# Kernel optimization log

Hardware: AMD Instinct MI355X
Metric: run time of the kernel (lower is better)

The kernel has to match this reference:

```python
import jax, jax.numpy as jnp
import numpy as np

N_NODES = 100000
N_EDGES = 1600000
DIM = 64


def setup_inputs() -> dict:
    key = jax.random.key(0)
    ks = jax.random.split(key, 10)
    return {
        "h_real": jax.random.normal(ks[0], (N_NODES, DIM), dtype=jnp.float32),
        "h_imag": jax.random.normal(ks[1], (N_NODES, DIM), dtype=jnp.float32),
        "d": jax.random.uniform(ks[2], (N_NODES,), dtype=jnp.float32),
        "w_real": jax.random.normal(ks[3], (N_EDGES,), dtype=jnp.float32),
        "w_imag": jax.random.normal(ks[4], (N_EDGES,), dtype=jnp.float32),
        "src": jax.random.randint(ks[5], (N_EDGES,), 0, N_NODES, dtype=jnp.int32),
        "dst": jax.random.randint(ks[6], (N_EDGES,), 0, N_NODES, dtype=jnp.int32),
        "W1": jax.random.normal(ks[7], (DIM, DIM), dtype=jnp.float32) * (1.414 / np.sqrt(DIM)),
        "b1": jnp.zeros((DIM,), dtype=jnp.float32),
        "W2": jax.random.normal(ks[8], (DIM, DIM), dtype=jnp.float32) * (1.414 / np.sqrt(DIM)),
        "b2": jnp.zeros((DIM,), dtype=jnp.float32),
    }


def reference(h_real, h_imag, d, w_real, w_imag, src, dst, W1, b1, W2, b2):
    n = h_real.shape[0]
    # per-edge complex coefficient e = d_dst * d_src * (w_real + i w_imag)
    dd = d[dst] * d[src]                      # [E]
    e_r = (dd * w_real)[:, None]              # [E,1]
    e_i = (dd * w_imag)[:, None]              # [E,1]
    hr = h_real[src]                          # [E,D]
    hi = h_imag[src]                          # [E,D]
    # complex multiply e * h, fused single pass over edges
    m_r = e_r * hr - e_i * hi                 # [E,D]
    m_i = e_i * hr + e_r * hi                 # [E,D]
    z_real = jax.ops.segment_sum(m_r, dst, num_segments=n)  # [N,D]
    z_imag = jax.ops.segment_sum(m_i, dst, num_segments=n)  # [N,D]
    # note: original overwrites z_real first, then z_imag uses the NEW z_real
    zr = (z_real @ W1.T + b1) - (z_imag @ W2.T + b2)
    zi = (zr @ W2.T + b2) + (z_imag @ W1.T + b1)
    return zr, zi
```

## Files before the change

### kernel.cpp

```cpp
#include <hip/hip_runtime.h>
#include <hip/hip_bf16.h>

#define N_NODES 100000
#define N_EDGES 1600000
#define DIM 64

#define K1 ((N_NODES + 255) / 256)
#define PACKB4 ((N_NODES * DIM / 4 + 255) / 256)
#define PTILE 8192
#define PARTB ((N_EDGES + PTILE - 1) / PTILE)
#define CAP 4480
#define QCAP 1344

typedef __attribute__((ext_vector_type(8))) short bf16x8;
typedef __attribute__((ext_vector_type(4))) float f32x4;

#if defined(__has_builtin)
#if __has_builtin(__builtin_amdgcn_fdot2_f32_bf16)
#define HAVE_DOT2 1
typedef __attribute__((ext_vector_type(2))) __bf16 bf16x2v;
#endif
#endif


__device__ __forceinline__ unsigned pack_bf16x2(float lo, float hi) {
  unsigned ulo = (unsigned)__hip_bfloat16_raw(__float2bfloat16(lo)).x;
  unsigned uhi = (unsigned)__hip_bfloat16_raw(__float2bfloat16(hi)).x;
  return ulo | (uhi << 16);
}
__device__ __forceinline__ float unpack_lo(unsigned u) {
  return __int_as_float((int)(u << 16));
}
__device__ __forceinline__ float unpack_hi(unsigned u) {
  return __int_as_float((int)(u & 0xFFFF0000u));
}
__device__ __forceinline__ unsigned short f2bf(float x) {
  return __hip_bfloat16_raw(__float2bfloat16(x)).x;
}

__global__ __launch_bounds__(256) void mega_kernel(
    const float* __restrict__ h_real, const float* __restrict__ h_imag,
    unsigned* __restrict__ hpack, const float* __restrict__ W1,
    const float* __restrict__ b1, const float* __restrict__ W2,
    const float* __restrict__ b2, unsigned short* __restrict__ At,
    float* __restrict__ cvec, const int* __restrict__ src,
    const int* __restrict__ dst, const float* __restrict__ dvec,
    const float* __restrict__ w_real, const float* __restrict__ w_imag,
    int* __restrict__ cursor, unsigned long long* __restrict__ records) {
  __shared__ __align__(16) float wstage[8192];
  const int bid = blockIdx.x;
  const int tid = threadIdx.x;

  if (bid < PACKB4) {
    const int i = bid * 256 + tid;
    const float4 hr = ((const float4*)h_real)[i];
    const float4 hi = ((const float4*)h_imag)[i];
    uint4 o;
    o.x = pack_bf16x2(hr.x, hi.x);
    o.y = pack_bf16x2(hr.y, hi.y);
    o.z = pack_bf16x2(hr.z, hi.z);
    o.w = pack_bf16x2(hr.w, hi.w);
    ((uint4*)hpack)[i] = o;
    return;
  }

  if (bid < PACKB4 + 64) {
    float* w1s = wstage;
    float* w2s = wstage + 4096;
    for (int i = tid; i < 64 * 64; i += 256) {
      w1s[i] = W1[i];
      w2s[i] = W2[i];
    }
    __syncthreads();
    const int idx = (bid - PACKB4) * 256 + tid;
    if (idx < 128 * 128) {
      const int n = idx >> 7, k = idx & 127;
      float v;
      if (n < 64) {
        v = (k < 64) ? w1s[n * 64 + k] : -w2s[n * 64 + (k - 64)];
      } else {
        const int nn = n - 64;
        if (k < 64) {
          float s = 0.0f;
          for (int j = 0; j < 64; ++j) s += w1s[j * 64 + k] * w2s[nn * 64 + j];
          v = s;
        } else {
          const int kk = k - 64;
          float s = 0.0f;
          for (int j = 0; j < 64; ++j) s += w2s[j * 64 + kk] * w2s[nn * 64 + j];
          v = w1s[nn * 64 + kk] - s;
        }
      }
      At[n * 128 + k] = f2bf(v);
    }
    if (idx < 128) {
      if (idx < 64) {
        cvec[idx] = b1[idx] - b2[idx];
      } else {
        const int nn = idx - 64;
        float s = 0.0f;
        for (int j = 0; j < 64; ++j) s += (b1[j] - b2[j]) * w2s[nn * 64 + j];
        cvec[idx] = s + b1[nn] + b2[nn];
      }
    }
    return;
  }

  int* lh = (int*)wstage;
  int* mybase = lh + K1;
  const int pb = bid - PACKB4 - 64;
  const int e0 = pb * PTILE;
  const int cnt_t = min(PTILE, N_EDGES - e0);

  for (int i = tid; i < K1; i += 256) lh[i] = 0;
  __syncthreads();

#pragma unroll
  for (int g = 0; g < PTILE / 1024; ++g) {
    const int off = g * 1024 + tid * 4;
    if (off < cnt_t) {
      const int4 t4 = *(const int4*)(dst + e0 + off);
      atomicAdd(&lh[t4.x >> 8], 1);
      atomicAdd(&lh[t4.y >> 8], 1);
      atomicAdd(&lh[t4.z >> 8], 1);
      atomicAdd(&lh[t4.w >> 8], 1);
    }
  }
  __syncthreads();

  for (int b = tid; b < K1; b += 256) {
    const int c = lh[b];
    mybase[b] = c ? atomicAdd(&cursor[b], c) : 0;
    lh[b] = 0;
  }
  __syncthreads();

#pragma unroll
  for (int g = 0; g < PTILE / 1024; ++g) {
    const int off = g * 1024 + tid * 4;
    if (off < cnt_t) {
      const int e = e0 + off;
      const int4 s4 = *(const int4*)(src + e);
      const int4 t4 = *(const int4*)(dst + e);
      const float4 wr = *(const float4*)(w_real + e);
      const float4 wi = *(const float4*)(w_imag + e);
#define EMIT(SS, TT, WR, WI)                                              \
      {                                                                   \
        const int b = (TT) >> 8;                                          \
        const float ds = dvec[SS];                                        \
        const unsigned lo = (unsigned)(SS) | ((unsigned)((TT) & 255) << 17); \
        const unsigned hi = pack_bf16x2(ds * (WR), ds * (WI));            \
        const int r = atomicAdd(&lh[b], 1);                               \
        const int pos = mybase[b] + r;                                    \
        if (pos < CAP)                                                    \
          records[(size_t)b * CAP + pos] =                                \
              ((unsigned long long)hi << 32) | lo;                        \
      }
      EMIT(s4.x, t4.x, wr.x, wi.x)
      EMIT(s4.y, t4.y, wr.y, wi.y)
      EMIT(s4.z, t4.z, wr.z, wi.z)
      EMIT(s4.w, t4.w, wr.w, wi.w)
#undef EMIT
    }
  }
}

__global__ __launch_bounds__(512, 8) void pull_sorted_kernel(
    const unsigned long long* __restrict__ records,
    const int* __restrict__ cursor, const float* __restrict__ dvec,
    const unsigned* __restrict__ hpack, const unsigned short* __restrict__ At,
    const float* __restrict__ cvec, float* __restrict__ zr_out,
    float* __restrict__ zi_out) {
  __shared__ unsigned long long stageB[QCAP];
  __shared__ __align__(16) unsigned short zs[64][136];
  __shared__ int ncnt[64];
  __shared__ int ncur[64];
  __shared__ int ns[64];
  __shared__ int ne[64];
  const int tid = threadIdx.x;
  const int lane = tid & 63;
  const int wave = tid >> 6;
  const int q4 = lane >> 4;
  const int m16 = lane & 15;
  const int b256 = blockIdx.x >> 2;
  const int qtr = blockIdx.x & 3;
  const int nbase = b256 * 256 + qtr * 64;
  const unsigned* __restrict__ hb = hpack + 4 * m16;

  const int bstart = b256 * CAP;
  const int bend = bstart + min(cursor[b256], CAP);

  if (tid < 64) ncnt[tid] = 0;
  __syncthreads();

  for (int i = bstart + tid; i < bend; i += 512) {
    const unsigned nl = ((unsigned)records[i] >> 17) & 255u;
    if ((int)(nl >> 6) == qtr) atomicAdd(&ncnt[nl & 63], 1);
  }
  __syncthreads();

  if (wave == 0) {
    const int c = ncnt[lane];
    int v = c;
#pragma unroll
    for (int off = 1; off < 64; off <<= 1) {
      int t = __shfl_up(v, off);
      if (lane >= off) v += t;
    }
    ns[lane] = v - c;
    ne[lane] = v;
    ncur[lane] = v - c;
  }
  __syncthreads();

  for (int i = bstart + tid; i < bend; i += 512) {
    const unsigned long long rec = records[i];
    const unsigned nl = ((unsigned)rec >> 17) & 255u;
    if ((int)(nl >> 6) == qtr) {
      const int pos = atomicAdd(&ncur[nl & 63], 1);
      if (pos < QCAP) stageB[pos] = rec;
    }
  }
  __syncthreads();

#if HAVE_DOT2
#define DOT2(acc, w_, h_)                                                   \
  acc = __builtin_amdgcn_fdot2_f32_bf16(__builtin_bit_cast(bf16x2v, (w_)),  \
                                        __builtin_bit_cast(bf16x2v, (h_)),  \
                                        acc, false)
#else
#define DOT2(acc, w_, h_)                                                   \
  {                                                                         \
    const float _wl = unpack_lo(w_), _wh = unpack_hi(w_);                   \
    const float _hl = unpack_lo(h_), _hh = unpack_hi(h_);                   \
    acc += _wl * _hl + _wh * _hh;                                           \
  }
#endif

#define GATH(RR) \
  (*reinterpret_cast<const uint4*>(hb + (size_t)((unsigned)(RR) & 0x1FFFF) * DIM))

#define DOTS(RR, HV)                                                        \
  {                                                                         \
    const unsigned cf = (unsigned)((RR) >> 32);                             \
    const unsigned wneg = cf ^ 0x80000000u;                                 \
    const unsigned wswp = (cf >> 16) | (cf << 16);                          \
    DOT2(sr0, wneg, (HV).x); DOT2(si0, wswp, (HV).x);                       \
    DOT2(sr1, wneg, (HV).y); DOT2(si1, wswp, (HV).y);                       \
    DOT2(sr2, wneg, (HV).z); DOT2(si2, wswp, (HV).z);                       \
    DOT2(sr3, wneg, (HV).w); DOT2(si3, wswp, (HV).w);                       \
  }

  for (int j = 0; j < 8; ++j) {
    const int l = wave * 8 + j;
    const int n = nbase + l;
    if (n >= N_NODES) break;
    const int s = min(ns[l], QCAP);
    const int e = min(ne[l], QCAP);
    const int deg = e - s;

    float sr0 = 0.f, sr1 = 0.f, sr2 = 0.f, sr3 = 0.f;
    float si0 = 0.f, si1 = 0.f, si2 = 0.f, si3 = 0.f;

    int p = s + q4;
    const int nfull = deg >> 2;
    int i = 0;
    for (; i + 4 <= nfull; i += 4) {
      const unsigned long long ra = stageB[p];
      const unsigned long long rb = stageB[p + 4];
      const unsigned long long rc = stageB[p + 8];
      const unsigned long long rd = stageB[p + 12];
      const uint4 ha = GATH(ra);
      const uint4 hbv = GATH(rb);
      const uint4 hc = GATH(rc);
      const uint4 hd = GATH(rd);
      DOTS(ra, ha) DOTS(rb, hbv) DOTS(rc, hc) DOTS(rd, hd)
      p += 16;
    }
    for (; i + 2 <= nfull; i += 2) {
      const unsigned long long ra = stageB[p];
      const unsigned long long rb = stageB[p + 4];
      const uint4 ha = GATH(ra);
      const uint4 hbv = GATH(rb);
      DOTS(ra, ha) DOTS(rb, hbv)
      p += 8;
    }
    if (i < nfull) {
      const unsigned long long ra = stageB[p];
      const uint4 ha = GATH(ra);
      DOTS(ra, ha)
      p += 4;
    }
    if (p < e) {
      const unsigned long long ra = stageB[p];
      const uint4 ha = GATH(ra);
      DOTS(ra, ha)
    }

#define QRED(v)                  \
    v += __shfl_xor(v, 16);      \
    v += __shfl_xor(v, 32);
    QRED(sr0) QRED(sr1) QRED(sr2) QRED(sr3)
    QRED(si0) QRED(si1) QRED(si2) QRED(si3)
#undef QRED

    const float dn = dvec[n];
    if (lane < 16) {
      uint2 rv, iv;
      rv.x = pack_bf16x2(dn * sr0, dn * sr1);
      rv.y = pack_bf16x2(dn * sr2, dn * sr3);
      iv.x = pack_bf16x2(dn * si0, dn * si1);
      iv.y = pack_bf16x2(dn * si2, dn * si3);
      *reinterpret_cast<uint2*>(&zs[l][4 * lane]) = rv;
      *reinterpret_cast<uint2*>(&zs[l][64 + 4 * lane]) = iv;
    }
  }
#undef DOTS
#undef GATH
#undef DOT2
  __syncthreads();

  {
    const int m = lane & 15;
    const int q = lane >> 4;
    const int ft = wave;
#pragma unroll
    for (int g = 0; g < 4; ++g) {
      bf16x8 a[4];
#pragma unroll
      for (int c = 0; c < 4; ++c)
        a[c] = *reinterpret_cast<const bf16x8*>(&zs[g * 16 + m][c * 32 + q * 8]);

      f32x4 acc = (f32x4){0.f, 0.f, 0.f, 0.f};
      const unsigned short* brow = At + (size_t)(ft * 16 + m) * 128 + q * 8;
#pragma unroll
      for (int c = 0; c < 4; ++c) {
        bf16x8 bfrag = *reinterpret_cast<const bf16x8*>(brow + c * 32);
        acc = __builtin_amdgcn_mfma_f32_16x16x32_bf16(a[c], bfrag, acc, 0, 0, 0);
      }

      const int nf = ft * 16 + m;
      const float bias = cvec[nf];
      float* outp = (nf < 64) ? zr_out : zi_out;
      const int nnn = nf & 63;
#pragma unroll
      for (int r = 0; r < 4; ++r) {
        const int node = nbase + g * 16 + q * 4 + r;
        if (node < N_NODES) outp[(size_t)node * 64 + nnn] = acc[r] + bias;
      }
    }
  }
}

extern "C" void kernel_launch(void* const* d_in, const int* in_sizes, int n_in,
                              void* d_out, int out_size, void* d_ws, size_t ws_size,
                              hipStream_t stream) {
  const float* h_real = (const float*)d_in[0];
  const float* h_imag = (const float*)d_in[1];
  const float* dvec   = (const float*)d_in[2];
  const float* w_real = (const float*)d_in[3];
  const float* w_imag = (const float*)d_in[4];
  const int*   src    = (const int*)d_in[5];
  const int*   dst    = (const int*)d_in[6];
  const float* W1     = (const float*)d_in[7];
  const float* b1     = (const float*)d_in[8];
  const float* W2     = (const float*)d_in[9];
  const float* b2     = (const float*)d_in[10];

  char* ws = (char*)d_ws;
  unsigned short* At = (unsigned short*)ws;
  float* cvec = (float*)(ws + 128 * 128 * 2);
  unsigned long long* records = (unsigned long long*)(ws + 33792);
  unsigned* hpack =
      (unsigned*)(ws + 33792 + (size_t)K1 * CAP * 8);
  int* cursor =
      (int*)(ws + 33792 + (size_t)K1 * CAP * 8 + (size_t)N_NODES * DIM * 4);

  float* zr_out = (float*)d_out;
  float* zi_out = zr_out + (size_t)N_NODES * DIM;

  hipMemsetAsync(cursor, 0, (size_t)K1 * sizeof(int), stream);
  mega_kernel<<<PACKB4 + 64 + PARTB, 256, 0, stream>>>(
      h_real, h_imag, (unsigned*)hpack, W1, b1, W2, b2, At, cvec,
      src, dst, dvec, w_real, w_imag, cursor, records);
  pull_sorted_kernel<<<K1 * 4, 512, 0, stream>>>(
      records, cursor, dvec, hpack, At, cvec, zr_out, zi_out);
}
```

Measured before the change: 287.2 us.

## Reorder fused-kernel block roles, shrink partition tiles, shrink LDS footprint

```diff
diff --git a/kernel.cpp b/kernel.cpp
--- a/kernel.cpp
+++ b/kernel.cpp
@@ -6,9 +6,10 @@
 #define DIM 64
 
 #define K1 ((N_NODES + 255) / 256)
-#define PACKB4 ((N_NODES * DIM / 4 + 255) / 256)
-#define PTILE 8192
+#define PTILE 2048
 #define PARTB ((N_EDGES + PTILE - 1) / PTILE)
+#define PACKV (N_NODES * DIM / 4)
+#define PACKB ((PACKV + 1023) / 1024)
 #define CAP 4480
 #define QCAP 1344
 
@@ -47,48 +48,88 @@
     const int* __restrict__ dst, const float* __restrict__ dvec,
     const float* __restrict__ w_real, const float* __restrict__ w_imag,
     int* __restrict__ cursor, unsigned long long* __restrict__ records) {
-  __shared__ __align__(16) float wstage[8192];
+  __shared__ int lh[K1];
+  __shared__ int mybase[K1];
   const int bid = blockIdx.x;
   const int tid = threadIdx.x;
 
-  if (bid < PACKB4) {
-    const int i = bid * 256 + tid;
-    const float4 hr = ((const float4*)h_real)[i];
-    const float4 hi = ((const float4*)h_imag)[i];
-    uint4 o;
-    o.x = pack_bf16x2(hr.x, hi.x);
-    o.y = pack_bf16x2(hr.y, hi.y);
-    o.z = pack_bf16x2(hr.z, hi.z);
-    o.w = pack_bf16x2(hr.w, hi.w);
-    ((uint4*)hpack)[i] = o;
+  if (bid < PARTB) {
+    const int e0 = bid * PTILE;
+    const int cnt_t = min(PTILE, N_EDGES - e0);
+
+    for (int i = tid; i < K1; i += 256) lh[i] = 0;
+    __syncthreads();
+
+#pragma unroll
+    for (int g = 0; g < PTILE / 1024; ++g) {
+      const int off = g * 1024 + tid * 4;
+      if (off < cnt_t) {
+        const int4 t4 = *(const int4*)(dst + e0 + off);
+        atomicAdd(&lh[t4.x >> 8], 1);
+        atomicAdd(&lh[t4.y >> 8], 1);
+        atomicAdd(&lh[t4.z >> 8], 1);
+        atomicAdd(&lh[t4.w >> 8], 1);
+      }
+    }
+    __syncthreads();
+
+    for (int b = tid; b < K1; b += 256) {
+      const int c = lh[b];
+      mybase[b] = c ? atomicAdd(&cursor[b], c) : 0;
+      lh[b] = 0;
+    }
+    __syncthreads();
+
+#pragma unroll
+    for (int g = 0; g < PTILE / 1024; ++g) {
+      const int off = g * 1024 + tid * 4;
+      if (off < cnt_t) {
+        const int e = e0 + off;
+        const int4 s4 = *(const int4*)(src + e);
+        const int4 t4 = *(const int4*)(dst + e);
+        const float4 wr = *(const float4*)(w_real + e);
+        const float4 wi = *(const float4*)(w_imag + e);
+#define EMIT(SS, TT, WR, WI)                                              \
+        {                                                                 \
+          const int b = (TT) >> 8;                                        \
+          const float ds = dvec[SS];                                      \
+          const unsigned lo =                                             \
+              (unsigned)(SS) | ((unsigned)((TT) & 255) << 17);            \
+          const unsigned hi = pack_bf16x2(ds * (WR), ds * (WI));          \
+          const int r = atomicAdd(&lh[b], 1);                             \
+          const int pos = mybase[b] + r;                                  \
+          if (pos < CAP)                                                  \
+            records[(size_t)b * CAP + pos] =                              \
+                ((unsigned long long)hi << 32) | lo;                      \
+        }
+        EMIT(s4.x, t4.x, wr.x, wi.x)
+        EMIT(s4.y, t4.y, wr.y, wi.y)
+        EMIT(s4.z, t4.z, wr.z, wi.z)
+        EMIT(s4.w, t4.w, wr.w, wi.w)
+#undef EMIT
+      }
+    }
     return;
   }
 
-  if (bid < PACKB4 + 64) {
-    float* w1s = wstage;
-    float* w2s = wstage + 4096;
-    for (int i = tid; i < 64 * 64; i += 256) {
-      w1s[i] = W1[i];
-      w2s[i] = W2[i];
-    }
-    __syncthreads();
-    const int idx = (bid - PACKB4) * 256 + tid;
+  if (bid < PARTB + 64) {
+    const int idx = (bid - PARTB) * 256 + tid;
     if (idx < 128 * 128) {
       const int n = idx >> 7, k = idx & 127;
       float v;
       if (n < 64) {
-        v = (k < 64) ? w1s[n * 64 + k] : -w2s[n * 64 + (k - 64)];
+        v = (k < 64) ? W1[n * 64 + k] : -W2[n * 64 + (k - 64)];
       } else {
         const int nn = n - 64;
         if (k < 64) {
           float s = 0.0f;
-          for (int j = 0; j < 64; ++j) s += w1s[j * 64 + k] * w2s[nn * 64 + j];
+          for (int j = 0; j < 64; ++j) s += W1[j * 64 + k] * W2[nn * 64 + j];
           v = s;
         } else {
           const int kk = k - 64;
           float s = 0.0f;
-          for (int j = 0; j < 64; ++j) s += w2s[j * 64 + kk] * w2s[nn * 64 + j];
-          v = w1s[nn * 64 + kk] - s;
+          for (int j = 0; j < 64; ++j) s += W2[j * 64 + kk] * W2[nn * 64 + j];
+          v = W1[nn * 64 + kk] - s;
         }
       }
       At[n * 128 + k] = f2bf(v);
@@ -99,68 +140,29 @@
       } else {
         const int nn = idx - 64;
         float s = 0.0f;
-        for (int j = 0; j < 64; ++j) s += (b1[j] - b2[j]) * w2s[nn * 64 + j];
+        for (int j = 0; j < 64; ++j) s += (b1[j] - b2[j]) * W2[nn * 64 + j];
         cvec[idx] = s + b1[nn] + b2[nn];
       }
     }
     return;
   }
 
-  int* lh = (int*)wstage;
-  int* mybase = lh + K1;
-  const int pb = bid - PACKB4 - 64;
-  const int e0 = pb * PTILE;
-  const int cnt_t = min(PTILE, N_EDGES - e0);
-
-  for (int i = tid; i < K1; i += 256) lh[i] = 0;
-  __syncthreads();
-
-#pragma unroll
-  for (int g = 0; g < PTILE / 1024; ++g) {
-    const int off = g * 1024 + tid * 4;
-    if (off < cnt_t) {
-      const int4 t4 = *(const int4*)(dst + e0 + off);
-      atomicAdd(&lh[t4.x >> 8], 1);
-      atomicAdd(&lh[t4.y >> 8], 1);
-      atomicAdd(&lh[t4.z >> 8], 1);
-      atomicAdd(&lh[t4.w >> 8], 1);
-    }
-  }
-  __syncthreads();
-
-  for (int b = tid; b < K1; b += 256) {
-    const int c = lh[b];
-    mybase[b] = c ? atomicAdd(&cursor[b], c) : 0;
-    lh[b] = 0;
-  }
-  __syncthreads();
-
-#pragma unroll
-  for (int g = 0; g < PTILE / 1024; ++g) {
-    const int off = g * 1024 + tid * 4;
-    if (off < cnt_t) {
-      const int e = e0 + off;
-      const int4 s4 = *(const int4*)(src + e);
-      const int4 t4 = *(const int4*)(dst + e);
-      const float4 wr = *(const float4*)(w_real + e);
-      const float4 wi = *(const float4*)(w_imag + e);
-#define EMIT(SS, TT, WR, WI)                                              \
-      {                                                                   \
-        const int b = (TT) >> 8;                                          \
-        const float ds = dvec[SS];                                        \
-        const unsigned lo = (unsigned)(SS) | ((unsigned)((TT) & 255) << 17); \
-        const unsigned hi = pack_bf16x2(ds * (WR), ds * (WI));            \
-        const int r = atomicAdd(&lh[b], 1);                               \
-        const int pos = mybase[b] + r;                                    \
-        if (pos < CAP)                                                    \
-          records[(size_t)b * CAP + pos] =                                \
-              ((unsigned long long)hi << 32) | lo;                        \
-      }
-      EMIT(s4.x, t4.x, wr.x, wi.x)
-      EMIT(s4.y, t4.y, wr.y, wi.y)
-      EMIT(s4.z, t4.z, wr.z, wi.z)
-      EMIT(s4.w, t4.w, wr.w, wi.w)
-#undef EMIT
+  {
+    const int pb = bid - PARTB - 64;
+    const int base = pb * 1024;
+#pragma unroll
+    for (int k = 0; k < 4; ++k) {
+      const int i = base + k * 256 + tid;
+      if (i < PACKV) {
+        const float4 hr = ((const float4*)h_real)[i];
+        const float4 hi = ((const float4*)h_imag)[i];
+        uint4 o;
+        o.x = pack_bf16x2(hr.x, hi.x);
+        o.y = pack_bf16x2(hr.y, hi.y);
+        o.z = pack_bf16x2(hr.z, hi.z);
+        o.w = pack_bf16x2(hr.w, hi.w);
+        ((uint4*)hpack)[i] = o;
+      }
     }
   }
 }
@@ -380,7 +382,7 @@
   float* zi_out = zr_out + (size_t)N_NODES * DIM;
 
   hipMemsetAsync(cursor, 0, (size_t)K1 * sizeof(int), stream);
-  mega_kernel<<<PACKB4 + 64 + PARTB, 256, 0, stream>>>(
+  mega_kernel<<<PARTB + 64 + PACKB, 256, 0, stream>>>(
       h_real, h_imag, (unsigned*)hpack, W1, b1, W2, b2, At, cvec,
       src, dst, dvec, w_real, w_imag, cursor, records);
   pull_sorted_kernel<<<K1 * 4, 512, 0, stream>>>(
```

Measured after the change: 264.3 us. 8.0% less time.
